# Performance work log

Measured on AMD Instinct MI355X. Metric: run time of the kernel, lower is better.

## Reference

```python
import jax, jax.numpy as jnp
import numpy as np

N_NODES = 50000
N_EDGES = 800000
IN_DIM = 64
HID = 64
NUM_GRAPHS = 512


def _gcn_conv(x, W, b, row, col, norm, n):
    # PyG GCNConv: h = x @ W; out[col] += norm * h[row]; out += b
    h = x @ W  # [N, HID]
    msg = h[row] * norm[:, None]  # [E', HID]
    out = jax.ops.segment_sum(msg, col, num_segments=n)
    return out + b


def setup_inputs() -> dict:
    key = jax.random.key(0)
    ks = jax.random.split(key, 12)
    x = jax.random.normal(ks[0], (N_NODES, IN_DIM), dtype=jnp.float32)
    edge_index = jax.random.randint(ks[1], (2, N_EDGES), 0, N_NODES, dtype=jnp.int64)
    batch = jnp.sort(jax.random.randint(ks[2], (N_NODES,), 0, NUM_GRAPHS, dtype=jnp.int64))
    s = 0.05
    W1 = jax.random.normal(ks[3], (IN_DIM, HID), dtype=jnp.float32) * s
    b1 = jnp.zeros((HID,), dtype=jnp.float32)
    W2 = jax.random.normal(ks[4], (HID, HID), dtype=jnp.float32) * s
    b2 = jnp.zeros((HID,), dtype=jnp.float32)
    W3 = jax.random.normal(ks[5], (HID, HID), dtype=jnp.float32) * s
    b3 = jnp.zeros((HID,), dtype=jnp.float32)
    lin_W = jax.random.normal(ks[6], (HID, 1), dtype=jnp.float32) * s
    lin_b = jnp.zeros((1,), dtype=jnp.float32)
    return {"x": x, "W1": W1, "b1": b1, "W2": W2, "b2": b2, "W3": W3,
            "b3": b3, "lin_W": lin_W, "lin_b": lin_b,
            "edge_index": edge_index, "batch": batch}


def reference(x, W1, b1, W2, b2, W3, b3, lin_W, lin_b, edge_index, batch):
    n = x.shape[0]
    # add self-loops (GCNConv default add_self_loops=True)
    loop = jnp.arange(n, dtype=edge_index.dtype)
    row = jnp.concatenate([edge_index[0], loop])  # source
    col = jnp.concatenate([edge_index[1], loop])  # target (aggregation index)
    # symmetric degree normalization: deg over targets with unit weights
    deg = jax.ops.segment_sum(jnp.ones_like(col, dtype=x.dtype), col, num_segments=n)
    dinv = jnp.where(deg > 0, jax.lax.rsqrt(deg), 0.0)
    norm = dinv[row] * dinv[col]  # [E+N]

    h = jax.nn.relu(_gcn_conv(x, W1, b1, row, col, norm, n))
    h = jax.nn.relu(_gcn_conv(h, W2, b2, row, col, norm, n))
    h = _gcn_conv(h, W3, b3, row, col, norm, n)

    # global_mean_pool over batch ids
    sums = jax.ops.segment_sum(h, batch, num_segments=NUM_GRAPHS)
    cnt = jax.ops.segment_sum(jnp.ones((n,), dtype=h.dtype), batch, num_segments=NUM_GRAPHS)
    pooled = sums / jnp.maximum(cnt, 1.0)[:, None]
    # dropout p=0.5 is identity in eval mode
    return pooled @ lin_W + lin_b  # [NUM_GRAPHS, 1]
```

## Files before the change

kernel.cpp:

```cpp
#include <hip/hip_runtime.h>
#include <hip/hip_fp16.h>

#define NN 50000
#define NE 800000
#define HD 64
#define NG 512
#define NBK 196
#define NBL 196
#define M_CNT (NBK * NBL)
#define NBS 151
#define GEMM_BLOCKS 3125


__global__ void zero_kernel(int* __restrict__ p, int n, int* __restrict__ q) {
    int i = blockIdx.x * blockDim.x + threadIdx.x;
    if (i < n) p[i] = 0;
    if (i < 64) q[i] = 0;
}

__global__ __launch_bounds__(256) void bucket_count(const int* __restrict__ col,
                                                    const int* __restrict__ batch,
                                                    int* __restrict__ counts,
                                                    int* __restrict__ beg,
                                                    int* __restrict__ endx) {
    __shared__ int hist[256];
    int tid = threadIdx.x, blk = blockIdx.x;
    hist[tid] = 0;
    __syncthreads();
    int base = blk * 4096;
#pragma unroll
    for (int k = 0; k < 16; ++k) {
        int e = base + k * 256 + tid;
        if (e < NE) atomicAdd(&hist[col[e] >> 8], 1);
    }
    int t = blk * 256 + tid;
    if (t < NN) {
        int g = batch[t];
        if (t == 0 || batch[t - 1] != g) beg[g] = t;
        if (t == NN - 1 || batch[t + 1] != g) endx[g] = t + 1;
    }
    __syncthreads();
    if (tid < NBK) counts[tid * NBL + blk] = hist[tid];
}

__global__ __launch_bounds__(256) void block_reduce(const int* __restrict__ src,
                                                    int* __restrict__ bsum) {
    __shared__ int ws[4];
    int tid = threadIdx.x, lane = tid & 63, wid = tid >> 6;
    int i = blockIdx.x * 256 + tid;
    int v = (i < M_CNT) ? src[i] : 0;
#pragma unroll
    for (int off = 32; off > 0; off >>= 1) v += __shfl_down(v, off, 64);
    if (lane == 0) ws[wid] = v;
    __syncthreads();
    if (tid == 0) bsum[blockIdx.x] = ws[0] + ws[1] + ws[2] + ws[3];
}

__global__ __launch_bounds__(64) void scan_bsum(int* __restrict__ bsum) {
    int lane = threadIdx.x;
    int carry = 0;
    for (int base = 0; base < NBS; base += 64) {
        int i = base + lane;
        int v = (i < NBS) ? bsum[i] : 0;
        int inc = v;
#pragma unroll
        for (int off = 1; off < 64; off <<= 1) {
            int t = __shfl_up(inc, off, 64);
            if (lane >= off) inc += t;
        }
        if (i < NBS) bsum[i] = carry + inc - v;
        carry += __shfl(inc, 63, 64);
    }
}

__global__ __launch_bounds__(256) void block_scan(const int* __restrict__ src,
                                                  const int* __restrict__ bsum,
                                                  int* __restrict__ dst) {
    __shared__ int ws[4];
    int tid = threadIdx.x, lane = tid & 63, wid = tid >> 6;
    int i = blockIdx.x * 256 + tid;
    int v = (i < M_CNT) ? src[i] : 0;
    int inc = v;
#pragma unroll
    for (int off = 1; off < 64; off <<= 1) {
        int t = __shfl_up(inc, off, 64);
        if (lane >= off) inc += t;
    }
    if (lane == 63) ws[wid] = inc;
    __syncthreads();
    int woff = 0;
    for (int k = 0; k < wid; ++k) woff += ws[k];
    if (i < M_CNT) dst[i] = bsum[blockIdx.x] + woff + inc - v;
}

__global__ __launch_bounds__(256) void gemm1_scatter(const float* __restrict__ x,
                                                     const float* __restrict__ W1,
                                                     __half* __restrict__ h16,
                                                     const int* __restrict__ row,
                                                     const int* __restrict__ col,
                                                     const int* __restrict__ counts_ex,
                                                     unsigned* __restrict__ packed) {
    if (blockIdx.x < GEMM_BLOCKS) {
        __shared__ float Ws[64][64];
        __shared__ float Is[16][64];
        int t = threadIdx.x;
        for (int i = t; i < 64 * 64; i += 256) Ws[i >> 6][i & 63] = W1[i];
        int row0 = blockIdx.x * 16;
        for (int i = t; i < 16 * 64; i += 256)
            Is[i >> 6][i & 63] = x[(row0 + (i >> 6)) * HD + (i & 63)];
        __syncthreads();
        int c = t & 63, r4 = t >> 6;
        float a0 = 0.f, a1 = 0.f, a2 = 0.f, a3 = 0.f;
#pragma unroll
        for (int k = 0; k < 64; ++k) {
            float w = Ws[k][c];
            a0 += Is[r4 + 0][k] * w;
            a1 += Is[r4 + 4][k] * w;
            a2 += Is[r4 + 8][k] * w;
            a3 += Is[r4 + 12][k] * w;
        }
        h16[(row0 + r4 + 0) * HD + c] = __float2half(a0);
        h16[(row0 + r4 + 4) * HD + c] = __float2half(a1);
        h16[(row0 + r4 + 8) * HD + c] = __float2half(a2);
        h16[(row0 + r4 + 12) * HD + c] = __float2half(a3);
    } else {
        __shared__ int cur[256];
        int tid = threadIdx.x, blk = blockIdx.x - GEMM_BLOCKS;
        cur[tid] = 0;
        __syncthreads();
        int base = blk * 4096;
#pragma unroll
        for (int k = 0; k < 16; ++k) {
            int e = base + k * 256 + tid;
            if (e < NE) {
                int c = col[e], r = row[e];
                int b = c >> 8;
                int lpos = atomicAdd(&cur[b], 1);
                int pos = counts_ex[b * NBL + blk] + lpos;
                packed[pos] = (unsigned)r | ((unsigned)(c & 255) << 16);
            }
        }
    }
}

__global__ __launch_bounds__(256) void csr_build(const unsigned* __restrict__ packed,
                                                 const int* __restrict__ counts_ex,
                                                 int* __restrict__ rowptr,
                                                 float* __restrict__ dinv,
                                                 int* __restrict__ esrc) {
    __shared__ int hist[256];
    __shared__ int ws[4];
    __shared__ int lrp[256];
    int bkt = blockIdx.x, tid = threadIdx.x;
    int s = counts_ex[bkt * NBL];
    int e = (bkt == NBK - 1) ? NE : counts_ex[(bkt + 1) * NBL];
    hist[tid] = 0;
    __syncthreads();
    for (int j = s + tid; j < e; j += 256)
        atomicAdd(&hist[(packed[j] >> 16) & 255], 1);
    __syncthreads();
    int lane = tid & 63, wid = tid >> 6;
    int v = hist[tid], inc = v;
#pragma unroll
    for (int off = 1; off < 64; off <<= 1) {
        int t = __shfl_up(inc, off, 64);
        if (lane >= off) inc += t;
    }
    if (lane == 63) ws[wid] = inc;
    __syncthreads();
    int woff = 0;
    for (int k = 0; k < wid; ++k) woff += ws[k];
    int excl = s + woff + inc - v;
    int node = bkt * 256 + tid;
    if (node < NN) {
        rowptr[node] = excl;
        dinv[node] = rsqrtf((float)(v + 1));
    }
    if (bkt == 0 && tid == 0) rowptr[NN] = NE;
    lrp[tid] = excl;
    hist[tid] = 0;
    __syncthreads();
    for (int j = s + tid; j < e; j += 256) {
        unsigned p = packed[j];
        int lc = (p >> 16) & 255;
        int slot = lrp[lc] + atomicAdd(&hist[lc], 1);
        esrc[slot] = (int)(p & 0xFFFF);
    }
}

__global__ __launch_bounds__(256) void gemm64_f16(const __half* __restrict__ in,
                                                  const float* __restrict__ W,
                                                  __half* __restrict__ out) {
    __shared__ float Ws[64][64];
    __shared__ float Is[16][64];
    int t = threadIdx.x;
    for (int i = t; i < 64 * 64; i += 256) Ws[i >> 6][i & 63] = W[i];
    int row0 = blockIdx.x * 16;
    const __half2* in2 = (const __half2*)(in + (size_t)row0 * HD);
    for (int i = t; i < 16 * 32; i += 256) {
        float2 v = __half22float2(in2[i]);
        int r = i >> 5, c2 = (i & 31) * 2;
        Is[r][c2]     = fmaxf(v.x, 0.f);
        Is[r][c2 + 1] = fmaxf(v.y, 0.f);
    }
    __syncthreads();
    int c = t & 63, r4 = t >> 6;
    float a0 = 0.f, a1 = 0.f, a2 = 0.f, a3 = 0.f;
#pragma unroll
    for (int k = 0; k < 64; ++k) {
        float w = Ws[k][c];
        a0 += Is[r4 + 0][k] * w;
        a1 += Is[r4 + 4][k] * w;
        a2 += Is[r4 + 8][k] * w;
        a3 += Is[r4 + 12][k] * w;
    }
    out[(row0 + r4 + 0) * HD + c] = __float2half(a0);
    out[(row0 + r4 + 4) * HD + c] = __float2half(a1);
    out[(row0 + r4 + 8) * HD + c] = __float2half(a2);
    out[(row0 + r4 + 12) * HD + c] = __float2half(a3);
}

template <bool POOL>
__global__ __launch_bounds__(256) void gather_sc(const __half* __restrict__ hp,
                                                 const int* __restrict__ rowptr,
                                                 const int* __restrict__ esrc,
                                                 const float* __restrict__ dinv,
                                                 const float* __restrict__ b,
                                                 __half* __restrict__ out16,
                                                 const int* __restrict__ batch,
                                                 float* __restrict__ pooled) {
    int tid = threadIdx.x, lane = tid & 63, wid = tid >> 6;
    int p = lane >> 5, c = lane & 31;
    int node = __builtin_amdgcn_readfirstlane(blockIdx.x * 4 + wid);
    const __half2* hv = (const __half2*)hp;
    int s = rowptr[node], e = rowptr[node + 1];
    float2 acc = {0.f, 0.f};
    int j = s;
    for (; j + 8 <= e; j += 8) {
        int s0 = esrc[j + 0], s1 = esrc[j + 1], s2 = esrc[j + 2], s3 = esrc[j + 3];
        int s4 = esrc[j + 4], s5 = esrc[j + 5], s6 = esrc[j + 6], s7 = esrc[j + 7];
        float w0 = dinv[s0], w1 = dinv[s1], w2 = dinv[s2], w3 = dinv[s3];
        float w4 = dinv[s4], w5 = dinv[s5], w6 = dinv[s6], w7 = dinv[s7];
        int a0 = p ? s1 : s0;  float u0 = p ? w1 : w0;
        int a1 = p ? s3 : s2;  float u1 = p ? w3 : w2;
        int a2 = p ? s5 : s4;  float u2 = p ? w5 : w4;
        int a3 = p ? s7 : s6;  float u3 = p ? w7 : w6;
        float2 f0 = __half22float2(hv[a0 * 32 + c]);
        float2 f1 = __half22float2(hv[a1 * 32 + c]);
        float2 f2 = __half22float2(hv[a2 * 32 + c]);
        float2 f3 = __half22float2(hv[a3 * 32 + c]);
        acc.x += u0 * f0.x + u1 * f1.x + u2 * f2.x + u3 * f3.x;
        acc.y += u0 * f0.y + u1 * f1.y + u2 * f2.y + u3 * f3.y;
    }
    for (; j < e; j += 2) {
        int s0 = esrc[j];
        int s1 = (j + 1 < e) ? esrc[j + 1] : s0;
        float w0 = dinv[s0];
        float w1 = (j + 1 < e) ? dinv[s1] : 0.f;
        int a = p ? s1 : s0;
        float u = p ? w1 : w0;
        float2 f = __half22float2(hv[a * 32 + c]);
        acc.x += u * f.x;
        acc.y += u * f.y;
    }
    acc.x += __shfl_xor(acc.x, 32, 64);
    acc.y += __shfl_xor(acc.y, 32, 64);
    if (p == 0) {
        float di = dinv[node];
        float2 self = __half22float2(hv[node * 32 + c]);
        float2 bb = ((const float2*)b)[c];
        float vx = di * acc.x + di * di * self.x + bb.x;
        float vy = di * acc.y + di * di * self.y + bb.y;
        if (POOL) {
            int g = batch[node];
            atomicAdd(&pooled[g * HD + 2 * c], vx);
            atomicAdd(&pooled[g * HD + 2 * c + 1], vy);
        } else {
            ((__half2*)out16)[node * 32 + c] = __floats2half2_rn(vx, vy);
        }
    }
}

__global__ __launch_bounds__(64) void final_kernel(const float* __restrict__ pooled,
                                                   const int* __restrict__ beg,
                                                   const int* __restrict__ endx,
                                                   const float* __restrict__ lin_W,
                                                   const float* __restrict__ lin_b,
                                                   float* __restrict__ out) {
    int g = blockIdx.x, d = threadIdx.x;
    float cnt = (float)(endx[g] - beg[g]);
    float v = pooled[g * HD + d] / fmaxf(cnt, 1.f) * lin_W[d];
#pragma unroll
    for (int off = 32; off > 0; off >>= 1) v += __shfl_down(v, off, 64);
    if (d == 0) out[g] = v + lin_b[0];
}

extern "C" void kernel_launch(void* const* d_in, const int* in_sizes, int n_in,
                              void* d_out, int out_size, void* d_ws, size_t ws_size,
                              hipStream_t stream) {
    const float* x     = (const float*)d_in[0];
    const float* W1    = (const float*)d_in[1];
    const float* b1    = (const float*)d_in[2];
    const float* W2    = (const float*)d_in[3];
    const float* b2    = (const float*)d_in[4];
    const float* W3    = (const float*)d_in[5];
    const float* b3    = (const float*)d_in[6];
    const float* lin_W = (const float*)d_in[7];
    const float* lin_b = (const float*)d_in[8];
    const int* edge_index = (const int*)d_in[9];
    const int* batch      = (const int*)d_in[10];
    const int* row = edge_index;
    const int* col = edge_index + NE;
    float* out = (float*)d_out;

    __half*   h16       = (__half*)d_ws;
    __half*   A16       = h16 + (size_t)NN * HD;
    int*      esrc      = (int*)(A16 + (size_t)NN * HD);
    unsigned* packed    = (unsigned*)(esrc + NE + 64);
    int*      counts    = (int*)(packed + NE);
    int*      counts_ex = counts + M_CNT;
    int*      rowptr    = counts_ex + M_CNT;
    float*    dinv      = (float*)(rowptr + NN + 2);
    int*      bsum      = (int*)(dinv + NN);
    float*    pooled    = (float*)(bsum + 256);
    int*      beg       = (int*)(pooled + NG * HD);
    int*      endx      = beg + NG;

    const int ZN = NG * HD + 2 * NG;
    zero_kernel<<<(ZN + 255) / 256, 256, 0, stream>>>((int*)pooled, ZN, esrc + NE);

    bucket_count<<<NBL, 256, 0, stream>>>(col, batch, counts, beg, endx);
    block_reduce<<<NBS, 256, 0, stream>>>(counts, bsum);
    scan_bsum<<<1, 64, 0, stream>>>(bsum);
    block_scan<<<NBS, 256, 0, stream>>>(counts, bsum, counts_ex);
    gemm1_scatter<<<GEMM_BLOCKS + NBL, 256, 0, stream>>>(x, W1, h16, row, col,
                                                         counts_ex, packed);
    csr_build<<<NBK, 256, 0, stream>>>(packed, counts_ex, rowptr, dinv, esrc);

    const int GB = NN / 4;

    gather_sc<false><<<GB, 256, 0, stream>>>(h16, rowptr, esrc, dinv, b1, A16,
                                             batch, pooled);
    gemm64_f16<<<GEMM_BLOCKS, 256, 0, stream>>>(A16, W2, h16);
    gather_sc<false><<<GB, 256, 0, stream>>>(h16, rowptr, esrc, dinv, b2, A16,
                                             batch, pooled);
    gemm64_f16<<<GEMM_BLOCKS, 256, 0, stream>>>(A16, W3, h16);
    gather_sc<true><<<GB, 256, 0, stream>>>(h16, rowptr, esrc, dinv, b3, nullptr,
                                            batch, pooled);

    final_kernel<<<NG, 64, 0, stream>>>(pooled, beg, endx, lin_W, lin_b, out);
}
```

Baseline: 269.3 us.

## Prescale features by source dinv to drop per-edge dinv gathers

Folds the source-side degree normalization into the feature rows before aggregation. The first GEMM now writes fp32, and csr_build converts it to fp16 scaled by dinv. The later GEMMs multiply their outputs by dinv, so each gather only sums features and then applies the target dinv. This removes one random dinv load per edge in all three gather passes, and the gather inner loop is unrolled to 16 edges. The zeroing kernel is folded into bucket_count, at the cost of an extra fp32 intermediate pass over the layer-1 features.

```diff
diff --git a/kernel.cpp b/kernel.cpp
--- a/kernel.cpp
+++ b/kernel.cpp
@@ -12,17 +12,12 @@
 #define GEMM_BLOCKS 3125
 
 
-__global__ void zero_kernel(int* __restrict__ p, int n, int* __restrict__ q) {
-    int i = blockIdx.x * blockDim.x + threadIdx.x;
-    if (i < n) p[i] = 0;
-    if (i < 64) q[i] = 0;
-}
-
 __global__ __launch_bounds__(256) void bucket_count(const int* __restrict__ col,
                                                     const int* __restrict__ batch,
                                                     int* __restrict__ counts,
                                                     int* __restrict__ beg,
-                                                    int* __restrict__ endx) {
+                                                    int* __restrict__ endx,
+                                                    float* __restrict__ pooled) {
     __shared__ int hist[256];
     int tid = threadIdx.x, blk = blockIdx.x;
     hist[tid] = 0;
@@ -34,6 +29,7 @@
         if (e < NE) atomicAdd(&hist[col[e] >> 8], 1);
     }
     int t = blk * 256 + tid;
+    if (t < NG * HD) pooled[t] = 0.f;
     if (t < NN) {
         int g = batch[t];
         if (t == 0 || batch[t - 1] != g) beg[g] = t;
@@ -95,7 +91,7 @@
 
 __global__ __launch_bounds__(256) void gemm1_scatter(const float* __restrict__ x,
                                                      const float* __restrict__ W1,
-                                                     __half* __restrict__ h16,
+                                                     float* __restrict__ h32,
                                                      const int* __restrict__ row,
                                                      const int* __restrict__ col,
                                                      const int* __restrict__ counts_ex,
@@ -119,10 +115,10 @@
             a2 += Is[r4 + 8][k] * w;
             a3 += Is[r4 + 12][k] * w;
         }
-        h16[(row0 + r4 + 0) * HD + c] = __float2half(a0);
-        h16[(row0 + r4 + 4) * HD + c] = __float2half(a1);
-        h16[(row0 + r4 + 8) * HD + c] = __float2half(a2);
-        h16[(row0 + r4 + 12) * HD + c] = __float2half(a3);
+        h32[(row0 + r4 + 0) * HD + c] = a0;
+        h32[(row0 + r4 + 4) * HD + c] = a1;
+        h32[(row0 + r4 + 8) * HD + c] = a2;
+        h32[(row0 + r4 + 12) * HD + c] = a3;
     } else {
         __shared__ int cur[256];
         int tid = threadIdx.x, blk = blockIdx.x - GEMM_BLOCKS;
@@ -147,10 +143,13 @@
                                                  const int* __restrict__ counts_ex,
                                                  int* __restrict__ rowptr,
                                                  float* __restrict__ dinv,
+                                                 const float* __restrict__ h32,
+                                                 __half* __restrict__ h16,
                                                  int* __restrict__ esrc) {
     __shared__ int hist[256];
     __shared__ int ws[4];
     __shared__ int lrp[256];
+    __shared__ float sdinv[256];
     int bkt = blockIdx.x, tid = threadIdx.x;
     int s = counts_ex[bkt * NBL];
     int e = (bkt == NBK - 1) ? NE : counts_ex[(bkt + 1) * NBL];
@@ -172,14 +171,26 @@
     for (int k = 0; k < wid; ++k) woff += ws[k];
     int excl = s + woff + inc - v;
     int node = bkt * 256 + tid;
+    float dv = rsqrtf((float)(v + 1));
     if (node < NN) {
         rowptr[node] = excl;
-        dinv[node] = rsqrtf((float)(v + 1));
+        dinv[node] = dv;
     }
     if (bkt == 0 && tid == 0) rowptr[NN] = NE;
     lrp[tid] = excl;
+    sdinv[tid] = dv;
     hist[tid] = 0;
     __syncthreads();
+    {
+        int nrows = (bkt == NBK - 1) ? (NN - 195 * 256) : 256;
+        const float2* hb32 = (const float2*)(h32 + (size_t)bkt * 256 * HD);
+        __half2* hb16 = (__half2*)(h16 + (size_t)bkt * 256 * HD);
+        for (int i = tid; i < nrows * 32; i += 256) {
+            float d = sdinv[i >> 5];
+            float2 f = hb32[i];
+            hb16[i] = __floats2half2_rn(d * f.x, d * f.y);
+        }
+    }
     for (int j = s + tid; j < e; j += 256) {
         unsigned p = packed[j];
         int lc = (p >> 16) & 255;
@@ -190,12 +201,15 @@
 
 __global__ __launch_bounds__(256) void gemm64_f16(const __half* __restrict__ in,
                                                   const float* __restrict__ W,
+                                                  const float* __restrict__ dinv,
                                                   __half* __restrict__ out) {
     __shared__ float Ws[64][64];
     __shared__ float Is[16][64];
+    __shared__ float sdinv[16];
     int t = threadIdx.x;
     for (int i = t; i < 64 * 64; i += 256) Ws[i >> 6][i & 63] = W[i];
     int row0 = blockIdx.x * 16;
+    if (t < 16) sdinv[t] = dinv[row0 + t];
     const __half2* in2 = (const __half2*)(in + (size_t)row0 * HD);
     for (int i = t; i < 16 * 32; i += 256) {
         float2 v = __half22float2(in2[i]);
@@ -214,14 +228,14 @@
         a2 += Is[r4 + 8][k] * w;
         a3 += Is[r4 + 12][k] * w;
     }
-    out[(row0 + r4 + 0) * HD + c] = __float2half(a0);
-    out[(row0 + r4 + 4) * HD + c] = __float2half(a1);
-    out[(row0 + r4 + 8) * HD + c] = __float2half(a2);
-    out[(row0 + r4 + 12) * HD + c] = __float2half(a3);
+    out[(row0 + r4 + 0) * HD + c] = __float2half(a0 * sdinv[r4 + 0]);
+    out[(row0 + r4 + 4) * HD + c] = __float2half(a1 * sdinv[r4 + 4]);
+    out[(row0 + r4 + 8) * HD + c] = __float2half(a2 * sdinv[r4 + 8]);
+    out[(row0 + r4 + 12) * HD + c] = __float2half(a3 * sdinv[r4 + 12]);
 }
 
 template <bool POOL>
-__global__ __launch_bounds__(256) void gather_sc(const __half* __restrict__ hp,
+__global__ __launch_bounds__(256) void gather_ns(const __half* __restrict__ hp,
                                                  const int* __restrict__ rowptr,
                                                  const int* __restrict__ esrc,
                                                  const float* __restrict__ dinv,
@@ -236,32 +250,38 @@
     int s = rowptr[node], e = rowptr[node + 1];
     float2 acc = {0.f, 0.f};
     int j = s;
-    for (; j + 8 <= e; j += 8) {
-        int s0 = esrc[j + 0], s1 = esrc[j + 1], s2 = esrc[j + 2], s3 = esrc[j + 3];
-        int s4 = esrc[j + 4], s5 = esrc[j + 5], s6 = esrc[j + 6], s7 = esrc[j + 7];
-        float w0 = dinv[s0], w1 = dinv[s1], w2 = dinv[s2], w3 = dinv[s3];
-        float w4 = dinv[s4], w5 = dinv[s5], w6 = dinv[s6], w7 = dinv[s7];
-        int a0 = p ? s1 : s0;  float u0 = p ? w1 : w0;
-        int a1 = p ? s3 : s2;  float u1 = p ? w3 : w2;
-        int a2 = p ? s5 : s4;  float u2 = p ? w5 : w4;
-        int a3 = p ? s7 : s6;  float u3 = p ? w7 : w6;
+    for (; j + 16 <= e; j += 16) {
+        int t0 = esrc[j + 0],  t1 = esrc[j + 1],  t2 = esrc[j + 2],  t3 = esrc[j + 3];
+        int t4 = esrc[j + 4],  t5 = esrc[j + 5],  t6 = esrc[j + 6],  t7 = esrc[j + 7];
+        int t8 = esrc[j + 8],  t9 = esrc[j + 9],  ta = esrc[j + 10], tb = esrc[j + 11];
+        int tc = esrc[j + 12], td = esrc[j + 13], te = esrc[j + 14], tf = esrc[j + 15];
+        int a0 = p ? t1 : t0;
+        int a1 = p ? t3 : t2;
+        int a2 = p ? t5 : t4;
+        int a3 = p ? t7 : t6;
+        int a4 = p ? t9 : t8;
+        int a5 = p ? tb : ta;
+        int a6 = p ? td : tc;
+        int a7 = p ? tf : te;
         float2 f0 = __half22float2(hv[a0 * 32 + c]);
         float2 f1 = __half22float2(hv[a1 * 32 + c]);
         float2 f2 = __half22float2(hv[a2 * 32 + c]);
         float2 f3 = __half22float2(hv[a3 * 32 + c]);
-        acc.x += u0 * f0.x + u1 * f1.x + u2 * f2.x + u3 * f3.x;
-        acc.y += u0 * f0.y + u1 * f1.y + u2 * f2.y + u3 * f3.y;
+        float2 f4 = __half22float2(hv[a4 * 32 + c]);
+        float2 f5 = __half22float2(hv[a5 * 32 + c]);
+        float2 f6 = __half22float2(hv[a6 * 32 + c]);
+        float2 f7 = __half22float2(hv[a7 * 32 + c]);
+        acc.x += (f0.x + f1.x) + (f2.x + f3.x) + (f4.x + f5.x) + (f6.x + f7.x);
+        acc.y += (f0.y + f1.y) + (f2.y + f3.y) + (f4.y + f5.y) + (f6.y + f7.y);
     }
     for (; j < e; j += 2) {
         int s0 = esrc[j];
         int s1 = (j + 1 < e) ? esrc[j + 1] : s0;
-        float w0 = dinv[s0];
-        float w1 = (j + 1 < e) ? dinv[s1] : 0.f;
         int a = p ? s1 : s0;
-        float u = p ? w1 : w0;
+        float valid = (p && j + 1 >= e) ? 0.f : 1.f;
         float2 f = __half22float2(hv[a * 32 + c]);
-        acc.x += u * f.x;
-        acc.y += u * f.y;
+        acc.x += valid * f.x;
+        acc.y += valid * f.y;
     }
     acc.x += __shfl_xor(acc.x, 32, 64);
     acc.y += __shfl_xor(acc.y, 32, 64);
@@ -269,8 +289,8 @@
         float di = dinv[node];
         float2 self = __half22float2(hv[node * 32 + c]);
         float2 bb = ((const float2*)b)[c];
-        float vx = di * acc.x + di * di * self.x + bb.x;
-        float vy = di * acc.y + di * di * self.y + bb.y;
+        float vx = di * (acc.x + self.x) + bb.x;
+        float vy = di * (acc.y + self.y) + bb.y;
         if (POOL) {
             int g = batch[node];
             atomicAdd(&pooled[g * HD + 2 * c], vx);
@@ -313,10 +333,11 @@
     const int* col = edge_index + NE;
     float* out = (float*)d_out;
 
-    __half*   h16       = (__half*)d_ws;
+    float*    h32       = (float*)d_ws;
+    __half*   h16       = (__half*)(h32 + (size_t)NN * HD);
     __half*   A16       = h16 + (size_t)NN * HD;
     int*      esrc      = (int*)(A16 + (size_t)NN * HD);
-    unsigned* packed    = (unsigned*)(esrc + NE + 64);
+    unsigned* packed    = (unsigned*)(esrc + NE);
     int*      counts    = (int*)(packed + NE);
     int*      counts_ex = counts + M_CNT;
     int*      rowptr    = counts_ex + M_CNT;
@@ -326,26 +347,24 @@
     int*      beg       = (int*)(pooled + NG * HD);
     int*      endx      = beg + NG;
 
-    const int ZN = NG * HD + 2 * NG;
-    zero_kernel<<<(ZN + 255) / 256, 256, 0, stream>>>((int*)pooled, ZN, esrc + NE);
-
-    bucket_count<<<NBL, 256, 0, stream>>>(col, batch, counts, beg, endx);
+    bucket_count<<<NBL, 256, 0, stream>>>(col, batch, counts, beg, endx, pooled);
     block_reduce<<<NBS, 256, 0, stream>>>(counts, bsum);
     scan_bsum<<<1, 64, 0, stream>>>(bsum);
     block_scan<<<NBS, 256, 0, stream>>>(counts, bsum, counts_ex);
-    gemm1_scatter<<<GEMM_BLOCKS + NBL, 256, 0, stream>>>(x, W1, h16, row, col,
+    gemm1_scatter<<<GEMM_BLOCKS + NBL, 256, 0, stream>>>(x, W1, h32, row, col,
                                                          counts_ex, packed);
-    csr_build<<<NBK, 256, 0, stream>>>(packed, counts_ex, rowptr, dinv, esrc);
+    csr_build<<<NBK, 256, 0, stream>>>(packed, counts_ex, rowptr, dinv,
+                                       h32, h16, esrc);
 
     const int GB = NN / 4;
 
-    gather_sc<false><<<GB, 256, 0, stream>>>(h16, rowptr, esrc, dinv, b1, A16,
+    gather_ns<false><<<GB, 256, 0, stream>>>(h16, rowptr, esrc, dinv, b1, A16,
                                              batch, pooled);
-    gemm64_f16<<<GEMM_BLOCKS, 256, 0, stream>>>(A16, W2, h16);
-    gather_sc<false><<<GB, 256, 0, stream>>>(h16, rowptr, esrc, dinv, b2, A16,
+    gemm64_f16<<<GEMM_BLOCKS, 256, 0, stream>>>(A16, W2, dinv, h16);
+    gather_ns<false><<<GB, 256, 0, stream>>>(h16, rowptr, esrc, dinv, b2, A16,
                                              batch, pooled);
-    gemm64_f16<<<GEMM_BLOCKS, 256, 0, stream>>>(A16, W3, h16);
-    gather_sc<true><<<GB, 256, 0, stream>>>(h16, rowptr, esrc, dinv, b3, nullptr,
+    gemm64_f16<<<GEMM_BLOCKS, 256, 0, stream>>>(A16, W3, dinv, h16);
+    gather_ns<true><<<GB, 256, 0, stream>>>(h16, rowptr, esrc, dinv, b3, nullptr,
                                             batch, pooled);
 
     final_kernel<<<NG, 64, 0, stream>>>(pooled, beg, endx, lin_W, lin_b, out);
```

After: 277.3 us. 1.03x slower.
